# Kernel optimization log

Hardware: AMD Instinct MI355X
Metric: run time of the kernel (lower is better)

## Reference

```python
import jax, jax.numpy as jnp
import numpy as np

P = 7          # corr_size (patch size)
PAD = P // 2   # displacement radius
PP = P * P     # 49 correlation channels
CHANS = [512, 1024, 512, 256, 256, 256]
HW = [64, 32, 16, 8, 4, 2]
B = 8


def _spatial_correlation(f1, f2):
    """out[b, pi*P+pj, y, x] = sum_c f1[b,c,y,x] * f2[b,c,y+pi-PAD, x+pj-PAD] (zero pad)."""
    Bb, C, H, W = f1.shape
    f2p = jnp.pad(f2, ((0, 0), (0, 0), (PAD, PAD), (PAD, PAD)))
    outs = [jnp.sum(f1 * f2p[:, :, di:di + H, dj:dj + W], axis=1)
            for di in range(P) for dj in range(P)]
    return jnp.stack(outs, axis=1)  # [B, P*P, H, W]


def _corr_lstm_cell(feat, feat_pre, h_pre, c_pre, w, b):
    corr = jax.nn.leaky_relu(_spatial_correlation(feat, feat_pre), 0.01)  # [B,49,H,W]
    lstm_in = jnp.concatenate([corr, h_pre], axis=1)                      # [B,98,H,W]
    conv = jax.lax.conv_general_dilated(
        lstm_in, w, window_strides=(1, 1), padding='SAME',
        dimension_numbers=('NCHW', 'OIHW', 'NCHW')) + b[None, :, None, None]
    cc_i, cc_f, cc_o, cc_g = jnp.split(conv, 4, axis=1)
    i = jax.nn.sigmoid(cc_i)
    f = jax.nn.sigmoid(cc_f)
    o = jax.nn.sigmoid(cc_o)
    g = jnp.tanh(cc_g)
    c_next = f * c_pre + i * g
    h_next = o * jnp.tanh(c_next)
    return h_next, c_next, corr


def setup_inputs() -> dict:
    key = jax.random.key(0)
    ks = jax.random.split(key, 6 * 6)
    d = {}
    ki = 0
    for l in range(6):
        C, S = CHANS[l], HW[l]
        d[f'x{l}'] = 0.05 * jax.random.normal(ks[ki], (B, C, S, S), jnp.float32); ki += 1
        d[f'xp{l}'] = 0.05 * jax.random.normal(ks[ki], (B, C, S, S), jnp.float32); ki += 1
        d[f'h{l}'] = 0.1 * jax.random.normal(ks[ki], (B, PP, S, S), jnp.float32); ki += 1
        d[f'c{l}'] = 0.1 * jax.random.normal(ks[ki], (B, PP, S, S), jnp.float32); ki += 1
        fan_in = 2 * PP * 9
        lim = float(np.sqrt(6.0 / (fan_in + 4 * PP * 9)))
        d[f'w{l}'] = jax.random.uniform(ks[ki], (4 * PP, 2 * PP, 3, 3), jnp.float32, -lim, lim); ki += 1
        bias = jnp.zeros((4 * PP,), jnp.float32).at[PP:2 * PP].set(1.0)  # forget-gate bias = 1
        d[f'b{l}'] = bias; ki += 1
    return d


def reference(x0, x1, x2, x3, x4, x5,
              xp0, xp1, xp2, xp3, xp4, xp5,
              h0, h1, h2, h3, h4, h5,
              c0, c1, c2, c3, c4, c5,
              w0, w1, w2, w3, w4, w5,
              b0, b1, b2, b3, b4, b5):
    xs = [x0, x1, x2, x3, x4, x5]
    xps = [xp0, xp1, xp2, xp3, xp4, xp5]
    hs = [h0, h1, h2, h3, h4, h5]
    cs = [c0, c1, c2, c3, c4, c5]
    ws = [w0, w1, w2, w3, w4, w5]
    bs = [b0, b1, b2, b3, b4, b5]
    outs = []
    for l in range(6):
        outs.append(_corr_lstm_cell(xs[l], xps[l], hs[l], cs[l], ws[l], bs[l]))
    h_next = tuple(o[0] for o in outs)
    c_next = tuple(o[1] for o in outs)
    corrs = tuple(o[2] for o in outs)
    return h_next + c_next + corrs  # flat 18-tuple
```

## Files before the change

### kernel.cpp

```cpp
#include <hip/hip_runtime.h>
#include <stdint.h>

#define DEV __device__ __forceinline__

typedef _Float16 half2_t __attribute__((ext_vector_type(2)));
typedef _Float16 half4_t __attribute__((ext_vector_type(4)));
typedef __bf16   bf16x8  __attribute__((ext_vector_type(8)));
typedef float    floatx4 __attribute__((ext_vector_type(4)));
typedef float    floatx2 __attribute__((ext_vector_type(2)));

DEV float fdot2f(half2_t a, half2_t b, float c) {
#if __has_builtin(__builtin_amdgcn_fdot2)
  return __builtin_amdgcn_fdot2(a, b, c, false);
#else
  return c + (float)a[0] * (float)b[0] + (float)a[1] * (float)b[1];
#endif
}

DEV half2_t pkh2(float a, float b) {
#if __has_builtin(__builtin_amdgcn_cvt_pkrtz)
  return __builtin_bit_cast(half2_t, __builtin_amdgcn_cvt_pkrtz(a, b));
#else
  half2_t r; r[0] = (_Float16)a; r[1] = (_Float16)b; return r;
#endif
}

DEV uint32_t f2bf(float f) {
  uint32_t u = __float_as_uint(f);
  return (u + 0x7FFFu + ((u >> 16) & 1u)) >> 16;
}

struct CorrCfg {
  const float* gx[6]; const float* gxp[6];
  int wg_start[3];
  int small_start[3];
  int S[3], C[3], tiles_x[3], tiles_pb[3], cpl[3];
  int sS[3], sC[3];
  long long poff[3], spoff[3];
};

template<int TH, int TWD>
__global__ __launch_bounds__(256)
void corr_kernel(CorrCfg cfg, _Float16* __restrict__ partial)
{
  int wg = blockIdx.x;
  if (wg >= cfg.small_start[0]) {
    int lvl = (wg >= cfg.small_start[2]) ? 2 : (wg >= cfg.small_start[1]) ? 1 : 0;
    long long i = (long long)(wg - cfg.small_start[lvl])*256 + threadIdx.x;
    const int S = cfg.sS[lvl], C = cfg.sC[lvl], SS = S*S;
    if (i >= (long long)8*49*SS) return;
    const float* X  = cfg.gx[lvl+3];
    const float* XP = cfg.gxp[lvl+3];
    int xc_ = (int)(i % S); int yc = (int)((i/S) % S);
    int d = (int)((i/SS) % 49); int b = (int)(i/((long long)49*SS));
    int yy = yc + d/7 - 3, xx = xc_ + (d%7) - 3;
    float s = 0.f;
    if (yy >= 0 && yy < S && xx >= 0 && xx < S) {
      const float* xb = X  + (size_t)b*C*SS + (size_t)yc*S + xc_;
      const float* pb = XP + (size_t)b*C*SS + (size_t)yy*S + xx;
      #pragma unroll 8
      for (int c = 0; c < C; ++c) s += xb[(size_t)c*SS] * pb[(size_t)c*SS];
    }
    partial[cfg.spoff[lvl] + i] = (_Float16)s;
    return;
  }
  constexpr int NT  = 256;
  constexpr int ROWS = TH + 6;
  constexpr int COLS = TWD + 6;
  constexpr int ST   = TWD + 7;
  constexpr int SLOTS = ROWS * 6 * 2;
  constexpr int PER   = (SLOTS + NT - 1)/NT;
  __shared__ half2_t ldsbuf[2][2][ROWS*ST] __attribute__((aligned(16)));

  int lvl = (wg >= cfg.wg_start[2]) ? 2 : (wg >= cfg.wg_start[1]) ? 1 : 0;
  wg -= cfg.wg_start[lvl];
  const float* X  = cfg.gx[lvl];
  const float* XP = cfg.gxp[lvl];
  const int S = cfg.S[lvl], C = cfg.C[lvl];
  const int txc = cfg.tiles_x[lvl], tpb = cfg.tiles_pb[lvl], cpl = cfg.cpl[lvl];
  const int per_split = 8 * tpb;
  const int sp = wg / per_split;
  const int rem = wg - sp*per_split;
  const int b = rem / tpb;
  const int t = rem - b*tpb;
  const int y0 = (t / txc) * TH, x0t = (t % txc) * TWD;
  const int tid = threadIdx.x;
  const int tx = tid & (TWD - 1), ty = tid / TWD;
  const int cbase = sp * cpl;
  const size_t SS = (size_t)S*S;
  const float* Xb  = X  + (size_t)b*C*SS;
  const float* XPb = XP + (size_t)b*C*SS;
  const int py = y0 + ty, px = x0t + tx;
  const size_t qoff = (size_t)py*S + px;

  int f_go[PER], f_base[PER], f_col0[PER], f_pr[PER];
  bool f_ok[PER], f_val[PER];
  #pragma unroll
  for (int s = 0; s < PER; ++s) {
    int i = tid + s*NT;
    bool val = (i < SLOTS);
    int ii = val ? i : 0;
    int pr = ii & 1;
    int rest = ii >> 1;
    int q = rest % 6;
    int r = rest / 6;
    int gy = y0 + r - 3;
    int gx0 = x0t - 4 + 4*q;
    bool ok = val && gy >= 0 && gy < S && gx0 >= 0 && (gx0 + 3) < S;
    f_val[s] = val; f_ok[s] = ok; f_pr[s] = pr;
    f_go[s] = ok ? gy*S + gx0 : 0;
    f_col0[s] = 4*q - 1;
    f_base[s] = r*ST;
  }

  float acc[49];
  #pragma unroll
  for (int d = 0; d < 49; ++d) acc[d] = 0.f;

  half2_t pk[PER][4];
  float xc[4], xn[4];

#define FILL_LOAD(c0v) { \
  _Pragma("unroll") for (int s = 0; s < PER; ++s) { \
    const float* p_ = XPb + (size_t)(cbase + (c0v) + 2*f_pr[s])*SS + f_go[s]; \
    floatx4 a_, b2_; \
    if (f_ok[s]) { a_ = *(const floatx4*)p_; b2_ = *(const floatx4*)(p_ + SS); } \
    else { a_ = (floatx4)0.f; b2_ = (floatx4)0.f; } \
    _Pragma("unroll") for (int j = 0; j < 4; ++j) \
      pk[s][j] = pkh2(a_[j], b2_[j]); } }

#define XLOAD(dst, c0v) { \
  _Pragma("unroll") for (int c = 0; c < 4; ++c) \
    dst[c] = Xb[(size_t)(cbase + (c0v) + c)*SS + qoff]; }

#define FILL_STORE(bbv) { \
  _Pragma("unroll") for (int s = 0; s < PER; ++s) if (f_val[s]) { \
    half2_t* plane_ = &ldsbuf[bbv][f_pr[s]][0]; \
    _Pragma("unroll") for (int j = 0; j < 4; ++j) { \
      int col_ = f_col0[s] + j; \
      if (col_ >= 0 && col_ < COLS) \
        plane_[f_base[s] + col_] = pk[s][j]; } } }

#define COMPUTE(bbv) { \
  _Pragma("unroll") for (int pr = 0; pr < 2; ++pr) { \
    half2_t xq = pkh2(xc[2*pr], xc[2*pr+1]); \
    _Pragma("unroll") for (int di = 0; di < 7; ++di) { \
      const half2_t* row_ = &ldsbuf[bbv][pr][(ty+di)*ST + tx]; \
      _Pragma("unroll") for (int dj = 0; dj < 7; ++dj) \
        acc[di*7+dj] = fdot2f(xq, row_[dj], acc[di*7+dj]); } } }

  const int nchunk = cpl >> 2;
  FILL_LOAD(0); XLOAD(xc, 0);
  FILL_STORE(0);
  FILL_LOAD(4); XLOAD(xn, 4);
  __syncthreads();
  for (int k = 0; k < nchunk; ++k) {
    const int bb = k & 1;
    if (k+1 < nchunk) FILL_STORE(bb^1);
    if (k+2 < nchunk) FILL_LOAD((k+2)*4);
    COMPUTE(bb);
    #pragma unroll
    for (int c = 0; c < 4; ++c) xc[c] = xn[c];
    if (k+2 < nchunk) XLOAD(xn, (k+2)*4);
    __syncthreads();
  }
#undef FILL_LOAD
#undef XLOAD
#undef FILL_STORE
#undef COMPUTE

  _Float16* P = partial + cfg.poff[lvl] + ((size_t)sp*8 + b)*49*SS + qoff;
  #pragma unroll
  for (int d = 0; d < 49; ++d) P[(size_t)d*SS] = (_Float16)acc[d];
}

__global__ __launch_bounds__(256)
void pack_w_kernel(const float* __restrict__ w0, const float* __restrict__ w1,
                   const float* __restrict__ w2, const float* __restrict__ w3,
                   const float* __restrict__ w4, const float* __restrict__ w5,
                   uint16_t* __restrict__ wpack)
{
  int idx = blockIdx.x*256 + threadIdx.x;
  int lvl = idx / 258048;
  int e = idx - lvl*258048;
  const float* W = lvl==0?w0:lvl==1?w1:lvl==2?w2:lvl==3?w3:lvl==4?w4:w5;
  int j = e & 7, lane = (e >> 3) & 63, rest = e >> 9;
  int s = rest % 36, tt = rest / 36;
  int n  = tt*16 + (lane & 15);
  int ch = (s & 3)*32 + (lane >> 4)*8 + j;
  int tap = s >> 2, ky = tap/3, kx = tap - 3*ky;
  float v = 0.f;
  if (n < 196 && ch < 98) v = W[((n*98 + ch)*3 + ky)*3 + kx];
  wpack[idx] = (uint16_t)f2bf(v);
}

struct P2Cfg {
  int blk_start[7];
  int S[6], nsplit[6], pxg[6], lg[6], gpb[6];
  long long poff[6], lstm_off[6], corr_off[6];
  const float* h[6];
};
__global__ __launch_bounds__(256)
void pass2_kernel(P2Cfg cfg, const _Float16* __restrict__ partial,
                  uint32_t* __restrict__ lstm, float* __restrict__ dout)
{
  __shared__ float lds[64*99];
  int blk = blockIdx.x;
  int lvl = 0;
  while (lvl < 5 && blk >= cfg.blk_start[lvl+1]) ++lvl;
  int rel = blk - cfg.blk_start[lvl];
  const int S = cfg.S[lvl], Sp = S + 2, SS = S*S;
  const int PXG = cfg.pxg[lvl], lg = cfg.lg[lvl], gpb = cfg.gpb[lvl];
  const int b = rel / gpb, g = rel - b*gpb;
  const int pixbase = g * PXG;
  const int tid = threadIdx.x;
  const int nsp = cfg.nsplit[lvl];
  const size_t spstride = (size_t)8*49*SS;
  for (int e = tid; e < PXG*98; e += 256) {
    int pxl = e & (PXG-1);
    int ch  = e >> lg;
    int pix = pixbase + pxl;
    float v;
    if (ch < 49) {
      const _Float16* P = partial + cfg.poff[lvl] + ((size_t)b*49 + ch)*SS + pix;
      float s = 0.f;
      for (int sp = 0; sp < nsp; ++sp) s += (float)P[(size_t)sp*spstride];
      s = s < 0.f ? 0.01f*s : s;
      dout[cfg.corr_off[lvl] + ((size_t)b*49 + ch)*SS + pix] = s;
      v = s;
    } else {
      v = cfg.h[lvl][((size_t)b*49 + (ch - 49))*SS + pix];
    }
    lds[pxl*99 + ch] = v;
  }
  __syncthreads();
  uint32_t* Lb = lstm + (cfg.lstm_off[lvl] >> 1);
  for (int f = tid; f < (PXG << 6); f += 256) {
    int pxl = f >> 6, c2 = f & 63;
    int pix = pixbase + pxl;
    int y = pix / S, x = pix - y*S;
    int c0 = 2*c2, c1 = c0 + 1;
    float v0 = c0 < 98 ? lds[pxl*99 + c0] : 0.f;
    float v1 = c1 < 98 ? lds[pxl*99 + c1] : 0.f;
    Lb[((size_t)(b*Sp + y + 1)*Sp + (x + 1))*64 + c2] = f2bf(v0) | (f2bf(v1) << 16);
  }
}

struct CCfg {
  int wg_start[7];
  int S[6], tiles_x[6], tiles_pb[6], lwsh[6], mfc[6], mgrp[6];
  long long lstm_off[6], wp_off[6], conv_off[6];
};
__global__ __launch_bounds__(256)
void conv_kernel(CCfg cfg, const uint16_t* __restrict__ lstm,
                 const uint16_t* __restrict__ wpack, float* __restrict__ cout)
{
  int wg = blockIdx.x;
  int lvl = 0;
  while (lvl < 5 && wg >= cfg.wg_start[lvl+1]) ++lvl;
  wg -= cfg.wg_start[lvl];
  const int S = cfg.S[lvl], Sp = S + 2;
  const int lwsh = cfg.lwsh[lvl], msk = (1 << lwsh) - 1;
  const int tpb = cfg.tiles_pb[lvl];
  const int b = wg / tpb, t = wg - b*tpb;
  const int ty0 = (t / cfg.tiles_x[lvl]) << (6 - lwsh);
  const int tx0 = (t % cfg.tiles_x[lvl]) << lwsh;
  const int wave = threadIdx.x >> 6, lane = threadIdx.x & 63;
  const int nhalf = wave & 1, mhalf = wave >> 1;
  const int mfc = cfg.mfc[lvl];
  if (mhalf >= cfg.mgrp[lvl]) return;
  const int mi = lane & 15, q = lane >> 4;
  const int SS = S*S;
  const uint16_t* lb = lstm + cfg.lstm_off[lvl] + (size_t)b*Sp*Sp*128;
  int aoff[2];
  #pragma unroll
  for (int mf = 0; mf < 2; ++mf) {
    int p = mhalf*32 + mf*16 + mi;
    int pc = p < SS ? p : 0;
    int y = ty0 + (pc >> lwsh), xx = tx0 + (pc & msk);
    aoff[mf] = (y*Sp + xx)*128 + q*8;
  }
  const uint16_t* wb = wpack + cfg.wp_off[lvl]
                     + (size_t)(nhalf*7)*36*512 + (size_t)lane*8;
  floatx4 acc[2][7];
  #pragma unroll
  for (int mf = 0; mf < 2; ++mf)
    #pragma unroll
    for (int nt = 0; nt < 7; ++nt) acc[mf][nt] = (floatx4)0.0f;

#define CONV_LOAD(sv, AV, BV) { \
  int tap_ = (sv) >> 2, cs_ = (sv) & 3; \
  int ky_ = tap_ / 3, kx_ = tap_ - 3*ky_; \
  int ao_ = ((ky_*Sp + kx_) << 7) + (cs_ << 5); \
  _Pragma("unroll") for (int mf = 0; mf < 2; ++mf) \
    if (mf < mfc) AV[mf] = *(const bf16x8*)(lb + aoff[mf] + ao_); \
  _Pragma("unroll") for (int nt = 0; nt < 7; ++nt) \
    BV[nt] = *(const bf16x8*)(wb + (size_t)((nt)*36 + (sv))*512); }

#define CONV_MFMA(AV, BV) { \
  _Pragma("unroll") for (int nt = 0; nt < 7; ++nt) \
    _Pragma("unroll") for (int mf = 0; mf < 2; ++mf) \
      if (mf < mfc) acc[mf][nt] = __builtin_amdgcn_mfma_f32_16x16x32_bf16( \
                        AV[mf], BV[nt], acc[mf][nt], 0, 0, 0); }

  bf16x8 av0[2], bv0[7], av1[2], bv1[7];
  CONV_LOAD(0, av0, bv0);
  for (int s = 0; s < 36; s += 2) {
    CONV_LOAD(s+1, av1, bv1);
    CONV_MFMA(av0, bv0);
    if (s+2 < 36) CONV_LOAD(s+2, av0, bv0);
    CONV_MFMA(av1, bv1);
  }
#undef CONV_LOAD
#undef CONV_MFMA

  float* co = cout + cfg.conv_off[lvl] + (size_t)b*196*SS;
  #pragma unroll
  for (int mf = 0; mf < 2; ++mf) {
    if (mf < mfc) {
      #pragma unroll
      for (int nt = 0; nt < 7; ++nt) {
        const int n = nhalf*112 + nt*16 + mi;
        if (n < 196) {
          #pragma unroll
          for (int r = 0; r < 4; ++r) {
            const int p = mhalf*32 + mf*16 + q*4 + r;
            if (p < SS) {
              const int y = ty0 + (p >> lwsh), xx = tx0 + (p & msk);
              co[(size_t)n*SS + y*S + xx] = acc[mf][nt][r];
            }
          }
        }
      }
    }
  }
}

struct GCfg {
  int blk_start[7];
  int S[6];
  long long conv_off[6], h_off[6], c_off[6];
  const float* cpre[6]; const float* bias[6];
};
__global__ __launch_bounds__(256)
void gate_kernel(GCfg cfg, const float* __restrict__ convout, float* __restrict__ dout)
{
  int blk = blockIdx.x;
  int lvl = 0;
  while (lvl < 5 && blk >= cfg.blk_start[lvl+1]) ++lvl;
  long long e = (long long)(blk - cfg.blk_start[lvl])*256 + threadIdx.x;
  const int S = cfg.S[lvl];
  const int SS = S*S;
  if (e >= (long long)8*49*SS) return;
  int b = (int)(e / ((long long)49*SS));
  int r1 = (int)(e - (long long)b*49*SS);
  int ch = r1 / SS;
  int p  = r1 - ch*SS;
  const float* cv = convout + cfg.conv_off[lvl] + ((size_t)b*196 + ch)*SS + p;
  const float* bb = cfg.bias[lvl];
  float ci  = cv[0]              + bb[ch];
  float cf  = cv[(size_t)49*SS]  + bb[ch+49];
  float co_ = cv[(size_t)98*SS]  + bb[ch+98];
  float cg  = cv[(size_t)147*SS] + bb[ch+147];
  float ig = 1.f/(1.f + __expf(-ci));
  float fg = 1.f/(1.f + __expf(-cf));
  float og = 1.f/(1.f + __expf(-co_));
  float g  = 1.f - 2.f/(__expf(2.f*cg) + 1.f);
  float cp = cfg.cpre[lvl][e];
  float cn = fg*cp + ig*g;
  float hn = og * (1.f - 2.f/(__expf(2.f*cn) + 1.f));
  dout[cfg.h_off[lvl] + e] = hn;
  dout[cfg.c_off[lvl] + e] = cn;
}

extern "C" void kernel_launch(void* const* d_in, const int* in_sizes, int n_in,
                              void* d_out, int out_size, void* d_ws, size_t ws_size,
                              hipStream_t stream)
{
  const float *x[6], *xp[6], *h[6], *cpre[6], *w[6], *bias[6];
  for (int l = 0; l < 6; ++l) {
    x[l]    = (const float*)d_in[6*l + 0];
    xp[l]   = (const float*)d_in[6*l + 1];
    h[l]    = (const float*)d_in[6*l + 2];
    cpre[l] = (const float*)d_in[6*l + 3];
    w[l]    = (const float*)d_in[6*l + 4];
    bias[l] = (const float*)d_in[6*l + 5];
  }
  static const int SL[6] = {64,32,16,8,4,2};
  static const int CL[6] = {512,1024,512,256,256,256};
  int NSPL[6] = {8,16,16,1,1,1};

  long long hsz[6], lstm_off[6], conv_off[6], h_off[6], poff[6];
  long long a1 = 0, a2 = 0, a3 = 0;
  for (int l = 0; l < 6; ++l) {
    int S = SL[l], Sp = S + 2;
    hsz[l] = 8LL*49*S*S;
    lstm_off[l] = a1; a1 += 8LL*Sp*Sp*128;
    conv_off[l] = a2; a2 += 8LL*196*S*S;
    h_off[l]    = a3; a3 += hsz[l];
  }
  long long pa = 0;
  for (int l = 0; l < 6; ++l) { poff[l] = pa; pa += (long long)NSPL[l]*hsz[l]; }
  {
    long long pr_bytes = (pa*2 > a2*4 ? pa*2 : a2*4);
    long long need = a1*2 + 6LL*258048*2 + pr_bytes;
    if (need > (long long)ws_size) {
      NSPL[0] = 4; NSPL[1] = 8; NSPL[2] = 16;
      pa = 0;
      for (int l = 0; l < 6; ++l) { poff[l] = pa; pa += (long long)NSPL[l]*hsz[l]; }
    }
  }
  const long long GRP = a3;
  const long long LSTM_ELEMS = a1;

  uint16_t* lstm  = (uint16_t*)d_ws;
  uint16_t* wpack = (uint16_t*)((char*)d_ws + LSTM_ELEMS*2);
  _Float16* partial = (_Float16*)((char*)d_ws + LSTM_ELEMS*2 + 6LL*258048*2);
  float* convout  = (float*)partial;
  float* dout = (float*)d_out;

  {
    CorrCfg ccfg;
    static const int tpb[3] = {16, 4, 1};
    static const int txx[3] = {4, 2, 1};
    for (int l = 0; l < 6; ++l) { ccfg.gx[l] = x[l]; ccfg.gxp[l] = xp[l]; }
    int start = 0;
    for (int l = 0; l < 3; ++l) {
      ccfg.wg_start[l] = start;
      ccfg.S[l] = SL[l]; ccfg.C[l] = CL[l];
      ccfg.tiles_x[l] = txx[l]; ccfg.tiles_pb[l] = tpb[l];
      ccfg.cpl[l] = CL[l]/NSPL[l];
      ccfg.poff[l] = poff[l];
      start += NSPL[l]*8*tpb[l];
    }
    for (int l = 0; l < 3; ++l) {
      ccfg.small_start[l] = start;
      ccfg.sS[l] = SL[l+3]; ccfg.sC[l] = CL[l+3];
      ccfg.spoff[l] = poff[l+3];
      start += (int)((hsz[l+3] + 255)/256);
    }
    corr_kernel<16,16><<<start, 256, 0, stream>>>(ccfg, partial);
  }
  (void)hipMemsetAsync(lstm, 0, (size_t)LSTM_ELEMS*2, stream);
  pack_w_kernel<<<6048, 256, 0, stream>>>(w[0],w[1],w[2],w[3],w[4],w[5], wpack);
  {
    P2Cfg p2; int start = 0;
    static const int PXGL[6] = {64,64,64,64,16,4};
    static const int LGL[6]  = {6,6,6,6,4,2};
    for (int l = 0; l < 6; ++l) {
      p2.blk_start[l] = start;
      int gpb = (SL[l]*SL[l]) / PXGL[l]; if (gpb < 1) gpb = 1;
      p2.gpb[l] = gpb;
      start += 8 * gpb;
      p2.S[l] = SL[l]; p2.nsplit[l] = NSPL[l];
      p2.pxg[l] = PXGL[l]; p2.lg[l] = LGL[l];
      p2.poff[l] = poff[l]; p2.lstm_off[l] = lstm_off[l];
      p2.corr_off[l] = 2*GRP + h_off[l];
      p2.h[l] = h[l];
    }
    p2.blk_start[6] = start;
    pass2_kernel<<<start, 256, 0, stream>>>(p2, partial, (uint32_t*)lstm, dout);
  }
  {
    CCfg cc;
    static const int ctpb[6] = {64, 16, 4, 1, 1, 1};
    static const int ctx[6]  = {4, 2, 1, 1, 1, 1};
    static const int clw[6]  = {4, 4, 4, 3, 2, 1};
    static const int cmfc[6] = {2, 2, 2, 2, 1, 1};
    static const int cmg[6]  = {2, 2, 2, 2, 1, 1};
    int start = 0;
    for (int l = 0; l < 6; ++l) {
      cc.wg_start[l] = start; start += 8*ctpb[l];
      cc.S[l] = SL[l]; cc.tiles_x[l] = ctx[l]; cc.tiles_pb[l] = ctpb[l];
      cc.lwsh[l] = clw[l]; cc.mfc[l] = cmfc[l]; cc.mgrp[l] = cmg[l];
      cc.lstm_off[l] = lstm_off[l];
      cc.wp_off[l] = 258048LL*l;
      cc.conv_off[l] = conv_off[l];
    }
    cc.wg_start[6] = start;
    conv_kernel<<<start, 256, 0, stream>>>(cc, lstm, wpack, convout);
  }
  {
    GCfg gc; int start = 0;
    for (int l = 0; l < 6; ++l) {
      gc.blk_start[l] = start;
      start += (int)((hsz[l] + 255)/256);
      gc.S[l] = SL[l];
      gc.conv_off[l] = conv_off[l];
      gc.h_off[l] = h_off[l];
      gc.c_off[l] = GRP + h_off[l];
      gc.cpre[l] = cpre[l];
      gc.bias[l] = bias[l];
    }
    gc.blk_start[6] = start;
    gate_kernel<<<start, 256, 0, stream>>>(gc, convout, dout);
  }
  (void)in_sizes; (void)n_in; (void)out_size; (void)ws_size;
}
```

Before: 524.1 us.

## Process two output pixels per thread in correlation kernel for large levels

```diff
diff --git a/kernel.cpp b/kernel.cpp
--- a/kernel.cpp
+++ b/kernel.cpp
@@ -32,21 +32,25 @@
 
 struct CorrCfg {
   const float* gx[6]; const float* gxp[6];
-  int wg_start[3];
+  int wg_start[2];
+  int mid_start;
   int small_start[3];
-  int S[3], C[3], tiles_x[3], tiles_pb[3], cpl[3];
+  int S[2], C[2], tiles_x[2], tiles_pb[2], cpl[2];
+  int mcpl;
   int sS[3], sC[3];
-  long long poff[3], spoff[3];
+  long long poff[2], mpoff, spoff[3];
 };
 
-template<int TH, int TWD>
 __global__ __launch_bounds__(256)
 void corr_kernel(CorrCfg cfg, _Float16* __restrict__ partial)
 {
+  __shared__ half2_t ldsbuf[2][2][22*40] __attribute__((aligned(16)));
+  const int tid = threadIdx.x;
   int wg = blockIdx.x;
+
   if (wg >= cfg.small_start[0]) {
     int lvl = (wg >= cfg.small_start[2]) ? 2 : (wg >= cfg.small_start[1]) ? 1 : 0;
-    long long i = (long long)(wg - cfg.small_start[lvl])*256 + threadIdx.x;
+    long long i = (long long)(wg - cfg.small_start[lvl])*256 + tid;
     const int S = cfg.sS[lvl], C = cfg.sC[lvl], SS = S*S;
     if (i >= (long long)8*49*SS) return;
     const float* X  = cfg.gx[lvl+3];
@@ -64,61 +68,158 @@
     partial[cfg.spoff[lvl] + i] = (_Float16)s;
     return;
   }
-  constexpr int NT  = 256;
-  constexpr int ROWS = TH + 6;
-  constexpr int COLS = TWD + 6;
-  constexpr int ST   = TWD + 7;
-  constexpr int SLOTS = ROWS * 6 * 2;
-  constexpr int PER   = (SLOTS + NT - 1)/NT;
-  __shared__ half2_t ldsbuf[2][2][ROWS*ST] __attribute__((aligned(16)));
-
-  int lvl = (wg >= cfg.wg_start[2]) ? 2 : (wg >= cfg.wg_start[1]) ? 1 : 0;
-  wg -= cfg.wg_start[lvl];
-  const float* X  = cfg.gx[lvl];
-  const float* XP = cfg.gxp[lvl];
-  const int S = cfg.S[lvl], C = cfg.C[lvl];
-  const int txc = cfg.tiles_x[lvl], tpb = cfg.tiles_pb[lvl], cpl = cfg.cpl[lvl];
-  const int per_split = 8 * tpb;
-  const int sp = wg / per_split;
-  const int rem = wg - sp*per_split;
-  const int b = rem / tpb;
-  const int t = rem - b*tpb;
-  const int y0 = (t / txc) * TH, x0t = (t % txc) * TWD;
-  const int tid = threadIdx.x;
-  const int tx = tid & (TWD - 1), ty = tid / TWD;
-  const int cbase = sp * cpl;
-  const size_t SS = (size_t)S*S;
-  const float* Xb  = X  + (size_t)b*C*SS;
-  const float* XPb = XP + (size_t)b*C*SS;
-  const int py = y0 + ty, px = x0t + tx;
-  const size_t qoff = (size_t)py*S + px;
-
-  int f_go[PER], f_base[PER], f_col0[PER], f_pr[PER];
-  bool f_ok[PER], f_val[PER];
-  #pragma unroll
-  for (int s = 0; s < PER; ++s) {
-    int i = tid + s*NT;
-    bool val = (i < SLOTS);
-    int ii = val ? i : 0;
-    int pr = ii & 1;
-    int rest = ii >> 1;
-    int q = rest % 6;
-    int r = rest / 6;
-    int gy = y0 + r - 3;
-    int gx0 = x0t - 4 + 4*q;
-    bool ok = val && gy >= 0 && gy < S && gx0 >= 0 && (gx0 + 3) < S;
-    f_val[s] = val; f_ok[s] = ok; f_pr[s] = pr;
-    f_go[s] = ok ? gy*S + gx0 : 0;
-    f_col0[s] = 4*q - 1;
-    f_base[s] = r*ST;
-  }
-
-  float acc[49];
-  #pragma unroll
-  for (int d = 0; d < 49; ++d) acc[d] = 0.f;
-
-  half2_t pk[PER][4];
-  float xc[4], xn[4];
+
+  if (wg >= cfg.mid_start) {
+    constexpr int NT = 256, MS = 16, MC = 512;
+    constexpr int ROWS = 22, COLS = 22, ST = 23;
+    constexpr int SLOTS = ROWS * 6 * 2;
+    constexpr int PER = 2;
+    int rel = wg - cfg.mid_start;
+    const int cpl = cfg.mcpl;
+    const int sp = rel >> 3;
+    const int b = rel & 7;
+    const int tx = tid & 15, ty = tid >> 4;
+    const int cbase = sp * cpl;
+    const size_t SS = (size_t)MS*MS;
+    const float* Xb  = cfg.gx[2]  + (size_t)b*MC*SS;
+    const float* XPb = cfg.gxp[2] + (size_t)b*MC*SS;
+    const size_t qoff = (size_t)ty*MS + tx;
+
+    int f_go[PER], f_base[PER], f_col0[PER], f_pr[PER];
+    bool f_ok[PER], f_val[PER];
+    #pragma unroll
+    for (int s = 0; s < PER; ++s) {
+      int i = tid + s*NT;
+      bool val = (i < SLOTS);
+      int ii = val ? i : 0;
+      int pr = ii & 1;
+      int rest = ii >> 1;
+      int q = rest % 6;
+      int r = rest / 6;
+      int gy = r - 3;
+      int gx0 = -4 + 4*q;
+      bool ok = val && gy >= 0 && gy < MS && gx0 >= 0 && (gx0 + 3) < MS;
+      f_val[s] = val; f_ok[s] = ok; f_pr[s] = pr;
+      f_go[s] = ok ? gy*MS + gx0 : 0;
+      f_col0[s] = 4*q - 1;
+      f_base[s] = r*ST;
+    }
+
+    float acc[49];
+    #pragma unroll
+    for (int d = 0; d < 49; ++d) acc[d] = 0.f;
+    half2_t pk[PER][4];
+    float xc[4], xn[4];
+
+#define MFILL_LOAD(c0v) { \
+  _Pragma("unroll") for (int s = 0; s < PER; ++s) { \
+    const float* p_ = XPb + (size_t)(cbase + (c0v) + 2*f_pr[s])*SS + f_go[s]; \
+    floatx4 a_, b2_; \
+    if (f_ok[s]) { a_ = *(const floatx4*)p_; b2_ = *(const floatx4*)(p_ + SS); } \
+    else { a_ = (floatx4)0.f; b2_ = (floatx4)0.f; } \
+    _Pragma("unroll") for (int j = 0; j < 4; ++j) \
+      pk[s][j] = pkh2(a_[j], b2_[j]); } }
+
+#define MXLOAD(dst, c0v) { \
+  _Pragma("unroll") for (int c = 0; c < 4; ++c) \
+    dst[c] = Xb[(size_t)(cbase + (c0v) + c)*SS + qoff]; }
+
+#define MFILL_STORE(bbv) { \
+  _Pragma("unroll") for (int s = 0; s < PER; ++s) if (f_val[s]) { \
+    half2_t* plane_ = &ldsbuf[bbv][f_pr[s]][0]; \
+    _Pragma("unroll") for (int j = 0; j < 4; ++j) { \
+      int col_ = f_col0[s] + j; \
+      if (col_ >= 0 && col_ < COLS) \
+        plane_[f_base[s] + col_] = pk[s][j]; } } }
+
+#define MCOMPUTE(bbv) { \
+  _Pragma("unroll") for (int pr = 0; pr < 2; ++pr) { \
+    half2_t xq = pkh2(xc[2*pr], xc[2*pr+1]); \
+    _Pragma("unroll") for (int di = 0; di < 7; ++di) { \
+      const half2_t* row_ = &ldsbuf[bbv][pr][(ty+di)*ST + tx]; \
+      _Pragma("unroll") for (int dj = 0; dj < 7; ++dj) \
+        acc[di*7+dj] = fdot2f(xq, row_[dj], acc[di*7+dj]); } } }
+
+    const int nchunk = cpl >> 2;
+    MFILL_LOAD(0); MXLOAD(xc, 0);
+    MFILL_STORE(0);
+    MFILL_LOAD(4); MXLOAD(xn, 4);
+    __syncthreads();
+    for (int k = 0; k < nchunk; ++k) {
+      const int bb = k & 1;
+      if (k+1 < nchunk) MFILL_STORE(bb^1);
+      if (k+2 < nchunk) MFILL_LOAD((k+2)*4);
+      MCOMPUTE(bb);
+      #pragma unroll
+      for (int c = 0; c < 4; ++c) xc[c] = xn[c];
+      if (k+2 < nchunk) MXLOAD(xn, (k+2)*4);
+      __syncthreads();
+    }
+#undef MFILL_LOAD
+#undef MXLOAD
+#undef MFILL_STORE
+#undef MCOMPUTE
+
+    _Float16* P = partial + cfg.mpoff + ((size_t)sp*8 + b)*49*SS + qoff;
+    #pragma unroll
+    for (int d = 0; d < 49; ++d) P[(size_t)d*SS] = (_Float16)acc[d];
+    return;
+  }
+
+  {
+    constexpr int NT = 256, TH = 16, TW = 32;
+    constexpr int ROWS = TH + 6;
+    constexpr int COLS = TW + 6;
+    constexpr int QUADS = 10;
+    constexpr int ST = TW + 8;
+    constexpr int SLOTS = ROWS * QUADS * 2;
+    constexpr int PER = 2;
+
+    int lvl = (wg >= cfg.wg_start[1]) ? 1 : 0;
+    wg -= cfg.wg_start[lvl];
+    const float* X  = cfg.gx[lvl];
+    const float* XP = cfg.gxp[lvl];
+    const int S = cfg.S[lvl], C = cfg.C[lvl];
+    const int txc = cfg.tiles_x[lvl], tpb = cfg.tiles_pb[lvl], cpl = cfg.cpl[lvl];
+    const int per_split = 8 * tpb;
+    const int sp = wg / per_split;
+    const int rem = wg - sp*per_split;
+    const int b = rem / tpb;
+    const int t = rem - b*tpb;
+    const int y0 = (t / txc) * TH, x0t = (t % txc) * TW;
+    const int tx = tid & 15, ty = tid >> 4;
+    const int cbase = sp * cpl;
+    const size_t SS = (size_t)S*S;
+    const float* Xb  = X  + (size_t)b*C*SS;
+    const float* XPb = XP + (size_t)b*C*SS;
+    const int py = y0 + ty, px = x0t + 2*tx;
+    const size_t qoff = (size_t)py*S + px;
+
+    int f_go[PER], f_base[PER], f_col0[PER], f_pr[PER];
+    bool f_ok[PER], f_val[PER];
+    #pragma unroll
+    for (int s = 0; s < PER; ++s) {
+      int i = tid + s*NT;
+      bool val = (i < SLOTS);
+      int ii = val ? i : 0;
+      int pr = ii & 1;
+      int rest = ii >> 1;
+      int q = rest % QUADS;
+      int r = rest / QUADS;
+      int gy = y0 + r - 3;
+      int gx0 = x0t - 4 + 4*q;
+      bool ok = val && gy >= 0 && gy < S && gx0 >= 0 && (gx0 + 3) < S;
+      f_val[s] = val; f_ok[s] = ok; f_pr[s] = pr;
+      f_go[s] = ok ? gy*S + gx0 : 0;
+      f_col0[s] = 4*q - 1;
+      f_base[s] = r*ST;
+    }
+
+    floatx2 acc[49];
+    #pragma unroll
+    for (int d = 0; d < 49; ++d) acc[d] = (floatx2)0.f;
+    half2_t pk[PER][4];
+    floatx2 xc[4], xn[4];
 
 #define FILL_LOAD(c0v) { \
   _Pragma("unroll") for (int s = 0; s < PER; ++s) { \
@@ -131,7 +232,7 @@
 
 #define XLOAD(dst, c0v) { \
   _Pragma("unroll") for (int c = 0; c < 4; ++c) \
-    dst[c] = Xb[(size_t)(cbase + (c0v) + c)*SS + qoff]; }
+    dst[c] = *(const floatx2*)(Xb + (size_t)(cbase + (c0v) + c)*SS + qoff); }
 
 #define FILL_STORE(bbv) { \
   _Pragma("unroll") for (int s = 0; s < PER; ++s) if (f_val[s]) { \
@@ -143,35 +244,46 @@
 
 #define COMPUTE(bbv) { \
   _Pragma("unroll") for (int pr = 0; pr < 2; ++pr) { \
-    half2_t xq = pkh2(xc[2*pr], xc[2*pr+1]); \
+    half2_t xqa = pkh2(xc[2*pr].x, xc[2*pr+1].x); \
+    half2_t xqb = pkh2(xc[2*pr].y, xc[2*pr+1].y); \
     _Pragma("unroll") for (int di = 0; di < 7; ++di) { \
-      const half2_t* row_ = &ldsbuf[bbv][pr][(ty+di)*ST + tx]; \
-      _Pragma("unroll") for (int dj = 0; dj < 7; ++dj) \
-        acc[di*7+dj] = fdot2f(xq, row_[dj], acc[di*7+dj]); } } }
-
-  const int nchunk = cpl >> 2;
-  FILL_LOAD(0); XLOAD(xc, 0);
-  FILL_STORE(0);
-  FILL_LOAD(4); XLOAD(xn, 4);
-  __syncthreads();
-  for (int k = 0; k < nchunk; ++k) {
-    const int bb = k & 1;
-    if (k+1 < nchunk) FILL_STORE(bb^1);
-    if (k+2 < nchunk) FILL_LOAD((k+2)*4);
-    COMPUTE(bb);
-    #pragma unroll
-    for (int c = 0; c < 4; ++c) xc[c] = xn[c];
-    if (k+2 < nchunk) XLOAD(xn, (k+2)*4);
+      const half2_t* row_ = &ldsbuf[bbv][pr][(ty+di)*ST + 2*tx]; \
+      half2_t L_[8]; \
+      _Pragma("unroll") for (int k = 0; k < 4; ++k) { \
+        half4_t v_ = *(const half4_t*)(row_ + 2*k); \
+        L_[2*k]   = __builtin_shufflevector(v_, v_, 0, 1); \
+        L_[2*k+1] = __builtin_shufflevector(v_, v_, 2, 3); } \
+      _Pragma("unroll") for (int dj = 0; dj < 7; ++dj) { \
+        acc[di*7+dj].x = fdot2f(xqa, L_[dj],   acc[di*7+dj].x); \
+        acc[di*7+dj].y = fdot2f(xqb, L_[dj+1], acc[di*7+dj].y); } } } }
+
+    const int nchunk = cpl >> 2;
+    FILL_LOAD(0); XLOAD(xc, 0);
+    FILL_STORE(0);
+    FILL_LOAD(4); XLOAD(xn, 4);
     __syncthreads();
-  }
+    for (int k = 0; k < nchunk; ++k) {
+      const int bb = k & 1;
+      if (k+1 < nchunk) FILL_STORE(bb^1);
+      if (k+2 < nchunk) FILL_LOAD((k+2)*4);
+      COMPUTE(bb);
+      #pragma unroll
+      for (int c = 0; c < 4; ++c) xc[c] = xn[c];
+      if (k+2 < nchunk) XLOAD(xn, (k+2)*4);
+      __syncthreads();
+    }
 #undef FILL_LOAD
 #undef XLOAD
 #undef FILL_STORE
 #undef COMPUTE
 
-  _Float16* P = partial + cfg.poff[lvl] + ((size_t)sp*8 + b)*49*SS + qoff;
-  #pragma unroll
-  for (int d = 0; d < 49; ++d) P[(size_t)d*SS] = (_Float16)acc[d];
+    _Float16* P = partial + cfg.poff[lvl] + ((size_t)sp*8 + b)*49*SS + qoff;
+    #pragma unroll
+    for (int d = 0; d < 49; ++d) {
+      half2_t pko = pkh2(acc[d].x, acc[d].y);
+      *(uint32_t*)(P + (size_t)d*SS) = *(const uint32_t*)&pko;
+    }
+  }
 }
 
 __global__ __launch_bounds__(256)
@@ -421,25 +533,29 @@
 
   {
     CorrCfg ccfg;
-    static const int tpb[3] = {16, 4, 1};
-    static const int txx[3] = {4, 2, 1};
+    static const int tpb2[2] = {8, 2};
+    static const int txx2[2] = {2, 1};
     for (int l = 0; l < 6; ++l) { ccfg.gx[l] = x[l]; ccfg.gxp[l] = xp[l]; }
     int start = 0;
-    for (int l = 0; l < 3; ++l) {
+    for (int l = 0; l < 2; ++l) {
       ccfg.wg_start[l] = start;
       ccfg.S[l] = SL[l]; ccfg.C[l] = CL[l];
-      ccfg.tiles_x[l] = txx[l]; ccfg.tiles_pb[l] = tpb[l];
+      ccfg.tiles_x[l] = txx2[l]; ccfg.tiles_pb[l] = tpb2[l];
       ccfg.cpl[l] = CL[l]/NSPL[l];
       ccfg.poff[l] = poff[l];
-      start += NSPL[l]*8*tpb[l];
-    }
+      start += NSPL[l]*8*tpb2[l];
+    }
+    ccfg.mid_start = start;
+    ccfg.mcpl = CL[2]/NSPL[2];
+    ccfg.mpoff = poff[2];
+    start += NSPL[2]*8;
     for (int l = 0; l < 3; ++l) {
       ccfg.small_start[l] = start;
       ccfg.sS[l] = SL[l+3]; ccfg.sC[l] = CL[l+3];
       ccfg.spoff[l] = poff[l+3];
       start += (int)((hsz[l+3] + 255)/256);
     }
-    corr_kernel<16,16><<<start, 256, 0, stream>>>(ccfg, partial);
+    corr_kernel<<<start, 256, 0, stream>>>(ccfg, partial);
   }
   (void)hipMemsetAsync(lstm, 0, (size_t)LSTM_ELEMS*2, stream);
   pack_w_kernel<<<6048, 256, 0, stream>>>(w[0],w[1],w[2],w[3],w[4],w[5], wpack);
```

New measurement: 504.1 us. 3.8% less time.
